# Optimization experiments

Hardware: AMD Instinct MI355X
Metric: run time of the kernel (lower is better)

Reference implementation:

```python
import jax, jax.numpy as jnp
import numpy as np

N1 = 50000
N2 = 50000
E = 800000
D = 128
DOUT = 128
L = 2
NEG_SLOPE = 0.2


def setup_inputs() -> dict:
    key = jax.random.key(0)
    ks = jax.random.split(key, 32)
    s = 0.05
    inp = {
        "x1": jax.random.normal(ks[0], (N1, D), jnp.float32),
        "x2": jax.random.normal(ks[1], (N2, D), jnp.float32),
        "ei11": jax.random.randint(ks[2], (2, E), 0, N1, jnp.int32),
        "ei22": jax.random.randint(ks[3], (2, E), 0, N2, jnp.int32),
        "ei12": jnp.stack([
            jax.random.randint(ks[4], (E,), 0, N1, jnp.int32),
            jax.random.randint(ks[5], (E,), 0, N2, jnp.int32),
        ]),
        # intra protein_1 GATConv params (shared lin for src/dst), stacked over layers
        "W_i1": jax.random.normal(ks[6], (L, D, D), jnp.float32) * s,
        "as_i1": jax.random.normal(ks[7], (L, D), jnp.float32) * s,
        "ad_i1": jax.random.normal(ks[8], (L, D), jnp.float32) * s,
        "b_i1": jnp.zeros((L, D), jnp.float32),
        # intra protein_2
        "W_i2": jax.random.normal(ks[9], (L, D, D), jnp.float32) * s,
        "as_i2": jax.random.normal(ks[10], (L, D), jnp.float32) * s,
        "ad_i2": jax.random.normal(ks[11], (L, D), jnp.float32) * s,
        "b_i2": jnp.zeros((L, D), jnp.float32),
        # inter protein_1 -> protein_2 (bipartite: separate src/dst lin)
        "Ws_x": jax.random.normal(ks[12], (L, D, D), jnp.float32) * s,
        "Wd_x": jax.random.normal(ks[13], (L, D, D), jnp.float32) * s,
        "as_x": jax.random.normal(ks[14], (L, D), jnp.float32) * s,
        "ad_x": jax.random.normal(ks[15], (L, D), jnp.float32) * s,
        "b_x": jnp.zeros((L, D), jnp.float32),
        # final linear
        "W_out": jax.random.normal(ks[16], (D, DOUT), jnp.float32) * s,
        "b_out": jnp.zeros((DOUT,), jnp.float32),
    }
    return inp


def _segment_softmax(logits, seg, num_segments):
    m = jax.ops.segment_max(logits, seg, num_segments=num_segments)
    e = jnp.exp(logits - m[seg])
    z = jax.ops.segment_sum(e, seg, num_segments=num_segments)
    return e / (z[seg] + 1e-16)


def _gat(x_src, x_dst, ei, W_src, W_dst, a_s, a_d, b, num_dst):
    hs = x_src @ W_src                       # [Ns, D]
    hd = x_dst @ W_dst                       # [Nd, D]
    src, dst = ei[0], ei[1]
    logit = jax.nn.leaky_relu((hs @ a_s)[src] + (hd @ a_d)[dst], NEG_SLOPE)  # [E]
    coef = _segment_softmax(logit, dst, num_dst)  # [E]
    out = jax.ops.segment_sum(coef[:, None] * hs[src], dst, num_segments=num_dst)
    return out + b


def reference(x1, x2, ei11, ei22, ei12, W_i1, as_i1, ad_i1, b_i1,
              W_i2, as_i2, ad_i2, b_i2, Ws_x, Wd_x, as_x, ad_x, b_x,
              W_out, b_out):
    h1, h2 = x1, x2
    for l in range(L):
        o1 = _gat(h1, h1, ei11, W_i1[l], W_i1[l], as_i1[l], ad_i1[l], b_i1[l], N1)
        o2 = _gat(h2, h2, ei22, W_i2[l], W_i2[l], as_i2[l], ad_i2[l], b_i2[l], N2)
        o2 = o2 + _gat(h1, h2, ei12, Ws_x[l], Wd_x[l], as_x[l], ad_x[l], b_x[l], N2)
        h1 = jax.nn.relu(o1)
        h2 = jax.nn.relu(o2)
    return (h1 @ W_out + b_out, h2 @ W_out + b_out)
```

## Files before the change

kernel.cpp:

```cpp
#include <hip/hip_runtime.h>
#include <hip/hip_bf16.h>
#include <hip/hip_fp16.h>
#include <cstdint>

#define D 128
#define NEG 0.2f
#define WSH 8
#define WIN 256
#define CAP 5120

typedef _Float16 f16x8 __attribute__((ext_vector_type(8)));
typedef float f32x4 __attribute__((ext_vector_type(4)));

static __device__ __forceinline__ ushort f2h(float x) {
  __half h = __float2half(x);
  return *reinterpret_cast<ushort*>(&h);
}
static __device__ __forceinline__ float h2f(ushort u) {
  __half h = *reinterpret_cast<__half*>(&u);
  return __half2float(h);
}

__global__ __launch_bounds__(256) void bin3_kernel(
    const int* __restrict__ ei0, const int* __restrict__ ei1, const int* __restrict__ ei2,
    int E0, int E1, int E2,
    int* __restrict__ p0, int* __restrict__ p1, int* __restrict__ p2,
    int* __restrict__ bcnt) {
  int sset = blockIdx.y;
  const int* ei = sset == 0 ? ei0 : (sset == 1 ? ei1 : ei2);
  int E = sset == 0 ? E0 : (sset == 1 ? E1 : E2);
  int* pairs = sset == 0 ? p0 : (sset == 1 ? p1 : p2);
  int* bc = bcnt + sset * 256;
  const int* src = ei;
  const int* dst = ei + E;
  __shared__ int lcnt[WIN], lcur[WIN], lbase[WIN];
  int t = threadIdx.x;
  lcnt[t] = 0; lcur[t] = 0;
  __syncthreads();
  int base = blockIdx.x * 2048;
  int s[8], d[8];
  #pragma unroll
  for (int k = 0; k < 8; k++) {
    int e = base + k * 256 + t;
    if (e < E) {
      s[k] = src[e]; d[k] = dst[e];
      atomicAdd(&lcnt[d[k] >> WSH], 1);
    } else d[k] = -1;
  }
  __syncthreads();
  if (lcnt[t] > 0) lbase[t] = atomicAdd(&bc[t], lcnt[t]);
  __syncthreads();
  #pragma unroll
  for (int k = 0; k < 8; k++) {
    if (d[k] >= 0) {
      int b = d[k] >> WSH;
      int r = atomicAdd(&lcur[b], 1);
      int slot = lbase[b] + r;
      if (slot < CAP)
        pairs[(size_t)b * CAP + slot] = (s[k] & 0xFFFF) | ((d[k] & 255) << 16);
    }
  }
}

__global__ __launch_bounds__(256) void count3_kernel(
    const int* __restrict__ p0, const int* __restrict__ p1, const int* __restrict__ p2,
    const int* __restrict__ bcnt,
    int* __restrict__ cnt0, int* __restrict__ cnt1, int* __restrict__ cnt2,
    int* __restrict__ off0, int* __restrict__ off1, int* __restrict__ off2,
    int* __restrict__ wsum, int N0, int N1, int N2) {
  int sset = blockIdx.y;
  const int* pairs = sset == 0 ? p0 : (sset == 1 ? p1 : p2);
  int* cnt = sset == 0 ? cnt0 : (sset == 1 ? cnt1 : cnt2);
  int* offs = sset == 0 ? off0 : (sset == 1 ? off1 : off2);
  int N = sset == 0 ? N0 : (sset == 1 ? N1 : N2);
  const int* bc = bcnt + sset * 256;
  int* ws = wsum + sset * 256;
  __shared__ int h[WIN];
  __shared__ int sc[WIN];
  int b = blockIdx.x, t = threadIdx.x;
  h[t] = 0; __syncthreads();
  int n = bc[b]; if (n > CAP) n = CAP;
  const int* p = pairs + (size_t)b * CAP;
  for (int i = t; i < n; i += 256) atomicAdd(&h[(p[i] >> 16) & 255], 1);
  __syncthreads();
  int v = h[t]; sc[t] = v; __syncthreads();
  for (int o = 1; o < 256; o <<= 1) {
    int x = (t >= o) ? sc[t - o] : 0; __syncthreads();
    sc[t] += x; __syncthreads();
  }
  int node = b * WIN + t;
  if (node < N) { cnt[node] = v; offs[node] = sc[t] - v; }
  if (t == 255) ws[b] = sc[255];
}

__global__ void wscan3_kernel(int* wsum) {
  __shared__ int sc[256];
  int t = threadIdx.x;
  int* w = wsum + blockIdx.x * 256;
  int v = w[t];
  sc[t] = v; __syncthreads();
  for (int o = 1; o < 256; o <<= 1) {
    int x = (t >= o) ? sc[t - o] : 0; __syncthreads();
    sc[t] += x; __syncthreads();
  }
  w[t] = sc[t] - v;
}

__global__ __launch_bounds__(256) void fill23_kernel(
    const int* __restrict__ p0, const int* __restrict__ p1, const int* __restrict__ p2,
    const int* __restrict__ bcnt, const int* __restrict__ wsum,
    int* __restrict__ off0, int* __restrict__ off1, int* __restrict__ off2,
    int* __restrict__ cs0, int* __restrict__ cs1, int* __restrict__ cs2,
    int N0, int N1, int N2) {
  int sset = blockIdx.y;
  const int* pairs = sset == 0 ? p0 : (sset == 1 ? p1 : p2);
  int* offs = sset == 0 ? off0 : (sset == 1 ? off1 : off2);
  int* csrc = sset == 0 ? cs0 : (sset == 1 ? cs1 : cs2);
  int N = sset == 0 ? N0 : (sset == 1 ? N1 : N2);
  const int* bc = bcnt + sset * 256;
  __shared__ int cur[WIN];
  int b = blockIdx.x, t = threadIdx.x;
  int wb = wsum[sset * 256 + b];
  int node = b * WIN + t;
  int start = 0;
  if (node < N) { start = offs[node] + wb; offs[node] = start; }
  cur[t] = start;
  __syncthreads();
  int n = bc[b]; if (n > CAP) n = CAP;
  const int* p = pairs + (size_t)b * CAP;
  for (int i = t; i < n; i += 256) {
    int v = p[i];
    int pp = atomicAdd(&cur[(v >> 16) & 255], 1);
    csrc[pp] = v & 0xFFFF;
  }
}

__global__ __launch_bounds__(256) void wprep6_kernel(
    const float* __restrict__ W_i1, const float* __restrict__ W_i2,
    const float* __restrict__ Ws_x,
    ushort* __restrict__ WtA, ushort* __restrict__ WtB, ushort* __restrict__ WtX) {
  int b = blockIdx.x;
  int which = b >> 1, l = b & 1;
  const float* Wb = (which == 0 ? W_i1 : (which == 1 ? W_i2 : Ws_x)) + l * 16384;
  ushort* Wo = (which == 0 ? WtA : (which == 1 ? WtB : WtX)) + l * 16384;
  __shared__ float s[128 * 129];
  int t = threadIdx.x;
  #pragma unroll
  for (int i = 0; i < 16; i++) {
    int idx = i * 256 + t;
    int k = idx >> 5, n4 = idx & 31;
    float4 v = *(const float4*)&Wb[k * 128 + n4 * 4];
    s[k * 129 + n4 * 4 + 0] = v.x;
    s[k * 129 + n4 * 4 + 1] = v.y;
    s[k * 129 + n4 * 4 + 2] = v.z;
    s[k * 129 + n4 * 4 + 3] = v.w;
  }
  __syncthreads();
  #pragma unroll
  for (int i = 0; i < 8; i++) {
    int idx = i * 256 + t;
    int n = idx >> 4, k8 = (idx & 15) * 8;
    ushort4 h0, h1;
    h0.x = f2h(s[(k8 + 0) * 129 + n]); h0.y = f2h(s[(k8 + 1) * 129 + n]);
    h0.z = f2h(s[(k8 + 2) * 129 + n]); h0.w = f2h(s[(k8 + 3) * 129 + n]);
    h1.x = f2h(s[(k8 + 4) * 129 + n]); h1.y = f2h(s[(k8 + 5) * 129 + n]);
    h1.z = f2h(s[(k8 + 6) * 129 + n]); h1.w = f2h(s[(k8 + 7) * 129 + n]);
    *(ushort4*)&Wo[n * 128 + k8] = h0;
    *(ushort4*)&Wo[n * 128 + k8 + 4] = h1;
  }
}

__global__ __launch_bounds__(256) void wprepout_kernel(
    const float* __restrict__ W, ushort* __restrict__ Wh, ushort* __restrict__ Wl) {
  __shared__ float s[128 * 129];
  int t = threadIdx.x;
  #pragma unroll
  for (int i = 0; i < 16; i++) {
    int idx = i * 256 + t;
    int k = idx >> 5, n4 = idx & 31;
    float4 v = *(const float4*)&W[k * 128 + n4 * 4];
    s[k * 129 + n4 * 4 + 0] = v.x;
    s[k * 129 + n4 * 4 + 1] = v.y;
    s[k * 129 + n4 * 4 + 2] = v.z;
    s[k * 129 + n4 * 4 + 3] = v.w;
  }
  __syncthreads();
  #pragma unroll
  for (int i = 0; i < 8; i++) {
    int idx = i * 256 + t;
    int n = idx >> 4, k8 = (idx & 15) * 8;
    ushort hh[8], ll[8];
    #pragma unroll
    for (int e = 0; e < 8; e++) {
      float w = s[(k8 + e) * 129 + n];
      hh[e] = f2h(w);
      ll[e] = f2h(w - h2f(hh[e]));
    }
    *(ushort4*)&Wh[n * 128 + k8]     = make_ushort4(hh[0], hh[1], hh[2], hh[3]);
    *(ushort4*)&Wh[n * 128 + k8 + 4] = make_ushort4(hh[4], hh[5], hh[6], hh[7]);
    *(ushort4*)&Wl[n * 128 + k8]     = make_ushort4(ll[0], ll[1], ll[2], ll[3]);
    *(ushort4*)&Wl[n * 128 + k8 + 4] = make_ushort4(ll[4], ll[5], ll[6], ll[7]);
  }
}

__global__ void wvec2_kernel(const float* __restrict__ Wd, const float* __restrict__ ad,
                             float* __restrict__ wv) {
  int l = blockIdx.x;
  int r = threadIdx.x;
  const float* Wb = Wd + (size_t)l * 16384;
  const float* ab = ad + l * 128;
  float s = 0.f;
  for (int c = 0; c < D; c++) s += Wb[r * D + c] * ab[c];
  wv[l * 128 + r] = s;
}

#define SWZ(b) ((b) ^ ((((b) >> 8) & 7) << 4))

template <int XF16>
__global__ __launch_bounds__(256) void gemm16_kernel(
    const void* __restrict__ Xv, const ushort* __restrict__ Wt,
    ushort* __restrict__ Yb,
    const float* __restrict__ a_sv, const float* __restrict__ a_dv,
    const float* __restrict__ wvec,
    float* __restrict__ aSo, float* __restrict__ aDo, float* __restrict__ aXo, int M) {
  __shared__ ushort sX[64 * 128];
  __shared__ ushort sW[128 * 128];
  __shared__ float sv[128];
  int t = threadIdx.x;
  int bm = blockIdx.x * 64;
  {
    const uint4* W4 = (const uint4*)Wt;
    #pragma unroll
    for (int i = 0; i < 8; i++) {
      int idx = i * 256 + t;
      int byte = idx * 16;
      *(uint4*)((char*)sW + SWZ(byte)) = W4[idx];
    }
  }
  {
    #pragma unroll
    for (int i = 0; i < 8; i++) {
      int idx = i * 256 + t;
      int row = idx >> 5, c4 = idx & 31;
      ushort4 h = make_ushort4(0, 0, 0, 0);
      if (bm + row < M) {
        if (XF16) {
          h = *(const ushort4*)((const ushort*)Xv + (size_t)(bm + row) * 128 + c4 * 4);
        } else {
          float4 v = ((const float4*)Xv)[(size_t)(bm + row) * 32 + c4];
          h.x = f2h(v.x); h.y = f2h(v.y); h.z = f2h(v.z); h.w = f2h(v.w);
        }
      }
      int byte = idx * 8;
      *(uint2*)((char*)sX + SWZ(byte)) = *(uint2*)&h;
    }
  }
  if (wvec != nullptr && t < 128) sv[t] = wvec[t];
  __syncthreads();

  int w = t >> 6, l = t & 63;
  int lq = l >> 4, lr = l & 15;
  int xrow = w * 16 + lr;
  f32x4 acc[8] = {};
  float ax = 0.f;
  #pragma unroll
  for (int kk = 0; kk < 4; kk++) {
    int xb = xrow * 256 + kk * 64 + lq * 16;
    f16x8 xa = *(const f16x8*)((const char*)sX + SWZ(xb));
    if (wvec != nullptr) {
      float4 w0 = *(const float4*)&sv[kk * 32 + lq * 8];
      float4 w1 = *(const float4*)&sv[kk * 32 + lq * 8 + 4];
      ax += (float)xa[0] * w0.x + (float)xa[1] * w0.y + (float)xa[2] * w0.z + (float)xa[3] * w0.w
          + (float)xa[4] * w1.x + (float)xa[5] * w1.y + (float)xa[6] * w1.z + (float)xa[7] * w1.w;
    }
    #pragma unroll
    for (int ct = 0; ct < 8; ct++) {
      int nb = (ct * 16 + lr) * 256 + kk * 64 + lq * 16;
      f16x8 wa = *(const f16x8*)((const char*)sW + SWZ(nb));
      acc[ct] = __builtin_amdgcn_mfma_f32_16x16x32_f16(wa, xa, acc[ct], 0, 0, 0);
    }
  }
  int row_m = bm + xrow;
  bool valid = row_m < M;
  #pragma unroll
  for (int ct = 0; ct < 8; ct++) {
    ushort4 h;
    h.x = f2h(acc[ct][0]); h.y = f2h(acc[ct][1]);
    h.z = f2h(acc[ct][2]); h.w = f2h(acc[ct][3]);
    if (valid) *(ushort4*)&Yb[(size_t)row_m * 128 + ct * 16 + lq * 4] = h;
  }
  if (a_sv != nullptr) {
    float s = 0.f;
    #pragma unroll
    for (int ct = 0; ct < 8; ct++) {
      float4 a = *(const float4*)&a_sv[ct * 16 + lq * 4];
      s += acc[ct][0] * a.x + acc[ct][1] * a.y + acc[ct][2] * a.z + acc[ct][3] * a.w;
    }
    s += __shfl_xor(s, 16); s += __shfl_xor(s, 32);
    if (valid && lq == 0) aSo[row_m] = s;
  }
  if (a_dv != nullptr) {
    float s = 0.f;
    #pragma unroll
    for (int ct = 0; ct < 8; ct++) {
      float4 a = *(const float4*)&a_dv[ct * 16 + lq * 4];
      s += acc[ct][0] * a.x + acc[ct][1] * a.y + acc[ct][2] * a.z + acc[ct][3] * a.w;
    }
    s += __shfl_xor(s, 16); s += __shfl_xor(s, 32);
    if (valid && lq == 0) aDo[row_m] = s;
  }
  if (wvec != nullptr) {
    ax += __shfl_xor(ax, 16); ax += __shfl_xor(ax, 32);
    if (valid && lq == 0) aXo[row_m] = ax;
  }
}

template <int XF16>
__global__ __launch_bounds__(256) void gemmx2_kernel(
    const void* __restrict__ Xv,
    const ushort* __restrict__ Wt0, const ushort* __restrict__ Wt1,
    ushort* __restrict__ Yb0, ushort* __restrict__ Yb1,
    const float* __restrict__ asv0, const float* __restrict__ asv1,
    const float* __restrict__ adv1,
    float* __restrict__ aSo0, float* __restrict__ aSo1, float* __restrict__ aDo1,
    int M) {
  int y = blockIdx.y;
  const ushort* Wt = y ? Wt1 : Wt0;
  ushort* Yb = y ? Yb1 : Yb0;
  const float* a_sv = y ? asv1 : asv0;
  const float* a_dv = y ? adv1 : nullptr;
  float* aSo = y ? aSo1 : aSo0;
  float* aDo = aDo1;
  __shared__ ushort sX[64 * 128];
  __shared__ ushort sW[128 * 128];
  int t = threadIdx.x;
  int bm = blockIdx.x * 64;
  {
    const uint4* W4 = (const uint4*)Wt;
    #pragma unroll
    for (int i = 0; i < 8; i++) {
      int idx = i * 256 + t;
      int byte = idx * 16;
      *(uint4*)((char*)sW + SWZ(byte)) = W4[idx];
    }
  }
  {
    #pragma unroll
    for (int i = 0; i < 8; i++) {
      int idx = i * 256 + t;
      int row = idx >> 5, c4 = idx & 31;
      ushort4 h = make_ushort4(0, 0, 0, 0);
      if (bm + row < M) {
        if (XF16) {
          h = *(const ushort4*)((const ushort*)Xv + (size_t)(bm + row) * 128 + c4 * 4);
        } else {
          float4 v = ((const float4*)Xv)[(size_t)(bm + row) * 32 + c4];
          h.x = f2h(v.x); h.y = f2h(v.y); h.z = f2h(v.z); h.w = f2h(v.w);
        }
      }
      int byte = idx * 8;
      *(uint2*)((char*)sX + SWZ(byte)) = *(uint2*)&h;
    }
  }
  __syncthreads();
  int w = t >> 6, l = t & 63;
  int lq = l >> 4, lr = l & 15;
  int xrow = w * 16 + lr;
  f32x4 acc[8] = {};
  #pragma unroll
  for (int kk = 0; kk < 4; kk++) {
    int xb = xrow * 256 + kk * 64 + lq * 16;
    f16x8 xa = *(const f16x8*)((const char*)sX + SWZ(xb));
    #pragma unroll
    for (int ct = 0; ct < 8; ct++) {
      int nb = (ct * 16 + lr) * 256 + kk * 64 + lq * 16;
      f16x8 wa = *(const f16x8*)((const char*)sW + SWZ(nb));
      acc[ct] = __builtin_amdgcn_mfma_f32_16x16x32_f16(wa, xa, acc[ct], 0, 0, 0);
    }
  }
  int row_m = bm + xrow;
  bool valid = row_m < M;
  #pragma unroll
  for (int ct = 0; ct < 8; ct++) {
    ushort4 h;
    h.x = f2h(acc[ct][0]); h.y = f2h(acc[ct][1]);
    h.z = f2h(acc[ct][2]); h.w = f2h(acc[ct][3]);
    if (valid) *(ushort4*)&Yb[(size_t)row_m * 128 + ct * 16 + lq * 4] = h;
  }
  {
    float s = 0.f;
    #pragma unroll
    for (int ct = 0; ct < 8; ct++) {
      float4 a = *(const float4*)&a_sv[ct * 16 + lq * 4];
      s += acc[ct][0] * a.x + acc[ct][1] * a.y + acc[ct][2] * a.z + acc[ct][3] * a.w;
    }
    s += __shfl_xor(s, 16); s += __shfl_xor(s, 32);
    if (valid && lq == 0) aSo[row_m] = s;
  }
  if (a_dv != nullptr) {
    float s = 0.f;
    #pragma unroll
    for (int ct = 0; ct < 8; ct++) {
      float4 a = *(const float4*)&a_dv[ct * 16 + lq * 4];
      s += acc[ct][0] * a.x + acc[ct][1] * a.y + acc[ct][2] * a.z + acc[ct][3] * a.w;
    }
    s += __shfl_xor(s, 16); s += __shfl_xor(s, 32);
    if (valid && lq == 0) aDo[row_m] = s;
  }
}

__global__ __launch_bounds__(512) void gemmfin_kernel(
    const float* __restrict__ XA, const float* __restrict__ XB,
    const ushort* __restrict__ Wh, const ushort* __restrict__ Wl,
    const float* __restrict__ bias,
    float* __restrict__ YA, float* __restrict__ YB, int MA, int MB, int mgA) {
  int bid = blockIdx.x;
  const float* X; float* Y; int M, bm;
  if (bid < mgA) { X = XA; Y = YA; M = MA; bm = bid * 128; }
  else           { X = XB; Y = YB; M = MB; bm = (bid - mgA) * 128; }
  __shared__ ushort sWh[128 * 128];
  __shared__ ushort sWl[128 * 128];
  __shared__ ushort sH[128 * 128];
  __shared__ ushort sL[128 * 128];
  int t = threadIdx.x;
  {
    const uint4* Wh4 = (const uint4*)Wh;
    const uint4* Wl4 = (const uint4*)Wl;
    #pragma unroll
    for (int i = 0; i < 4; i++) {
      int idx = i * 512 + t;
      int byte = idx * 16;
      *(uint4*)((char*)sWh + SWZ(byte)) = Wh4[idx];
      *(uint4*)((char*)sWl + SWZ(byte)) = Wl4[idx];
    }
  }
  {
    const float4* X4 = (const float4*)X;
    #pragma unroll
    for (int i = 0; i < 8; i++) {
      int idx = i * 512 + t;
      int row = idx >> 5, c4 = idx & 31;
      float4 v = make_float4(0.f, 0.f, 0.f, 0.f);
      if (bm + row < M) v = X4[(size_t)(bm + row) * 32 + c4];
      ushort4 h, lo;
      h.x = f2h(v.x); lo.x = f2h(v.x - h2f(h.x));
      h.y = f2h(v.y); lo.y = f2h(v.y - h2f(h.y));
      h.z = f2h(v.z); lo.z = f2h(v.z - h2f(h.z));
      h.w = f2h(v.w); lo.w = f2h(v.w - h2f(h.w));
      int byte = idx * 8;
      *(uint2*)((char*)sH + SWZ(byte)) = *(uint2*)&h;
      *(uint2*)((char*)sL + SWZ(byte)) = *(uint2*)&lo;
    }
  }
  __syncthreads();
  int w = t >> 6, l = t & 63;
  int lq = l >> 4, lr = l & 15;
  int xrow = w * 16 + lr;
  f32x4 acc[8] = {};
  #pragma unroll
  for (int kk = 0; kk < 4; kk++) {
    int xb = xrow * 256 + kk * 64 + lq * 16;
    f16x8 xh = *(const f16x8*)((const char*)sH + SWZ(xb));
    f16x8 xl = *(const f16x8*)((const char*)sL + SWZ(xb));
    #pragma unroll
    for (int ct = 0; ct < 8; ct++) {
      int nb = (ct * 16 + lr) * 256 + kk * 64 + lq * 16;
      f16x8 wh = *(const f16x8*)((const char*)sWh + SWZ(nb));
      f16x8 wl = *(const f16x8*)((const char*)sWl + SWZ(nb));
      acc[ct] = __builtin_amdgcn_mfma_f32_16x16x32_f16(wh, xh, acc[ct], 0, 0, 0);
      acc[ct] = __builtin_amdgcn_mfma_f32_16x16x32_f16(wl, xh, acc[ct], 0, 0, 0);
      acc[ct] = __builtin_amdgcn_mfma_f32_16x16x32_f16(wh, xl, acc[ct], 0, 0, 0);
    }
  }
  int row_m = bm + xrow;
  if (row_m < M) {
    #pragma unroll
    for (int ct = 0; ct < 8; ct++) {
      float4 b = *(const float4*)&bias[ct * 16 + lq * 4];
      float4 o = make_float4(acc[ct][0] + b.x, acc[ct][1] + b.y,
                             acc[ct][2] + b.z, acc[ct][3] + b.w);
      *(float4*)&Y[(size_t)row_m * 128 + ct * 16 + lq * 4] = o;
    }
  }
}

template <int F16O>
__global__ __launch_bounds__(256) void agg_kernel(
    const ushort* __restrict__ hs, const float* __restrict__ aS, const float* __restrict__ aD,
    const int* __restrict__ offs, const int* __restrict__ cnt, const int* __restrict__ csrc,
    const void* __restrict__ prevv, const float* __restrict__ bias1,
    const float* __restrict__ bias2, void* __restrict__ outv, int N, int dorelu) {
  int wid = threadIdx.x >> 6, lane = threadIdx.x & 63;
  int d = blockIdx.x * 4 + wid;
  if (d >= N) return;
  int st = offs[d], deg = cnt[d];
  float adv = aD[d];
  int quarter = lane >> 4;
  int q = lane & 15;
  float acc[8] = {};
  float z = 0.f;
  for (int base = 0; base < deg; base += 64) {
    int m = deg - base; if (m > 64) m = 64;
    int sidx = 0; float el = 0.f;
    if (lane < m) {
      sidx = csrc[st + base + lane];
      float l = aS[sidx] + adv;
      l = (l > 0.f) ? l : NEG * l;
      el = __expf(l);
    }
    float zs = el;
    for (int o = 32; o > 0; o >>= 1) zs += __shfl_xor(zs, o);
    z += zs;
    #pragma unroll 4
    for (int j = 0; j < m; j += 4) {
      int jj = j + quarter;
      int sj = __shfl(sidx, jj);
      float ej = __shfl(el, jj);
      uint4 hv = *(const uint4*)(hs + (size_t)sj * D + q * 8);
      float2 f0 = __half22float2(*reinterpret_cast<__half2*>(&hv.x));
      float2 f1 = __half22float2(*reinterpret_cast<__half2*>(&hv.y));
      float2 f2 = __half22float2(*reinterpret_cast<__half2*>(&hv.z));
      float2 f3 = __half22float2(*reinterpret_cast<__half2*>(&hv.w));
      acc[0] += ej * f0.x; acc[1] += ej * f0.y;
      acc[2] += ej * f1.x; acc[3] += ej * f1.y;
      acc[4] += ej * f2.x; acc[5] += ej * f2.y;
      acc[6] += ej * f3.x; acc[7] += ej * f3.y;
    }
  }
  #pragma unroll
  for (int k = 0; k < 8; k++) {
    acc[k] += __shfl_xor(acc[k], 16);
    acc[k] += __shfl_xor(acc[k], 32);
  }
  if (quarter == 0) {
    float inv = 1.f / (z + 1e-16f);
    float o[8];
    #pragma unroll
    for (int k = 0; k < 8; k++) o[k] = acc[k] * inv;
    size_t rb = (size_t)d * D + q * 8;
    if (prevv) {
      if (F16O) {
        uint4 pv = *(const uint4*)((const ushort*)prevv + rb);
        float2 p0 = __half22float2(*reinterpret_cast<__half2*>(&pv.x));
        float2 p1 = __half22float2(*reinterpret_cast<__half2*>(&pv.y));
        float2 p2 = __half22float2(*reinterpret_cast<__half2*>(&pv.z));
        float2 p3 = __half22float2(*reinterpret_cast<__half2*>(&pv.w));
        o[0]+=p0.x; o[1]+=p0.y; o[2]+=p1.x; o[3]+=p1.y;
        o[4]+=p2.x; o[5]+=p2.y; o[6]+=p3.x; o[7]+=p3.y;
      } else {
        const float* prev = (const float*)prevv;
        float4 p0 = *(const float4*)(prev + rb);
        float4 p1 = *(const float4*)(prev + rb + 4);
        o[0]+=p0.x; o[1]+=p0.y; o[2]+=p0.z; o[3]+=p0.w;
        o[4]+=p1.x; o[5]+=p1.y; o[6]+=p1.z; o[7]+=p1.w;
      }
    }
    if (bias1) {
      float4 b0 = *(const float4*)(bias1 + q * 8);
      float4 b1 = *(const float4*)(bias1 + q * 8 + 4);
      o[0]+=b0.x; o[1]+=b0.y; o[2]+=b0.z; o[3]+=b0.w;
      o[4]+=b1.x; o[5]+=b1.y; o[6]+=b1.z; o[7]+=b1.w;
    }
    if (bias2) {
      float4 b0 = *(const float4*)(bias2 + q * 8);
      float4 b1 = *(const float4*)(bias2 + q * 8 + 4);
      o[0]+=b0.x; o[1]+=b0.y; o[2]+=b0.z; o[3]+=b0.w;
      o[4]+=b1.x; o[5]+=b1.y; o[6]+=b1.z; o[7]+=b1.w;
    }
    if (dorelu) {
      #pragma unroll
      for (int k = 0; k < 8; k++) o[k] = o[k] > 0.f ? o[k] : 0.f;
    }
    if (F16O) {
      ushort4 u0 = make_ushort4(f2h(o[0]), f2h(o[1]), f2h(o[2]), f2h(o[3]));
      ushort4 u1 = make_ushort4(f2h(o[4]), f2h(o[5]), f2h(o[6]), f2h(o[7]));
      *(ushort4*)((ushort*)outv + rb)     = u0;
      *(ushort4*)((ushort*)outv + rb + 4) = u1;
    } else {
      float* out = (float*)outv;
      *(float4*)(out + rb)     = make_float4(o[0], o[1], o[2], o[3]);
      *(float4*)(out + rb + 4) = make_float4(o[4], o[5], o[6], o[7]);
    }
  }
}

extern "C" void kernel_launch(void* const* d_in, const int* in_sizes, int n_in,
                              void* d_out, int out_size, void* d_ws, size_t ws_size,
                              hipStream_t stream) {
  const float* x1   = (const float*)d_in[0];
  const float* x2   = (const float*)d_in[1];
  const int*   ei11 = (const int*)d_in[2];
  const int*   ei22 = (const int*)d_in[3];
  const int*   ei12 = (const int*)d_in[4];
  const float* W_i1 = (const float*)d_in[5];
  const float* as_i1= (const float*)d_in[6];
  const float* ad_i1= (const float*)d_in[7];
  const float* b_i1 = (const float*)d_in[8];
  const float* W_i2 = (const float*)d_in[9];
  const float* as_i2= (const float*)d_in[10];
  const float* ad_i2= (const float*)d_in[11];
  const float* b_i2 = (const float*)d_in[12];
  const float* Ws_x = (const float*)d_in[13];
  const float* Wd_x = (const float*)d_in[14];
  const float* as_x = (const float*)d_in[15];
  const float* ad_x = (const float*)d_in[16];
  const float* b_x  = (const float*)d_in[17];
  const float* W_out= (const float*)d_in[18];
  const float* b_out= (const float*)d_in[19];

  int N1 = in_sizes[0] / D, N2 = in_sizes[1] / D;
  int E11 = in_sizes[2] / 2, E22 = in_sizes[3] / 2, E12 = in_sizes[4] / 2;
  int Nmax = (N1 > N2) ? N1 : N2;
  int Emax = E11 > E22 ? (E11 > E12 ? E11 : E12) : (E22 > E12 ? E22 : E12);
  int NB1 = (N1 + WIN - 1) / WIN, NB2 = (N2 + WIN - 1) / WIN;
  int NBmax = (NB1 > NB2) ? NB1 : NB2;

  float* outA = (float*)d_out;
  float* outB = outA + (size_t)N1 * D;

  char* w = (char*)d_ws;
  auto alloc = [&](size_t b) { char* p = w; w += (b + 255) & ~(size_t)255; return p; };
  size_t pair_bytes = (size_t)NBmax * CAP * 4;
  size_t hsmax = (size_t)Nmax * D * 2;
  ushort* BB  = (ushort*)alloc(hsmax > pair_bytes ? hsmax : pair_bytes);
  ushort* BX  = (ushort*)alloc(hsmax > pair_bytes ? hsmax : pair_bytes);
  ushort* h1  = (ushort*)alloc(((size_t)N1 * D * 2) > pair_bytes ? ((size_t)N1 * D * 2) : pair_bytes);
  ushort* h2  = (ushort*)alloc((size_t)N2 * D * 2);
  int* pairs0 = (int*)BB;
  int* pairs1 = (int*)BX;
  int* pairs2 = (int*)h1;
  float* aS   = (float*)alloc((size_t)Nmax * 4);
  float* aD   = (float*)alloc((size_t)Nmax * 4);
  float* aDx  = (float*)alloc((size_t)Nmax * 4);
  float* aS2  = (float*)alloc((size_t)Nmax * 4);
  float* wvecB= (float*)alloc(256 * 4);
  ushort* WtA = (ushort*)alloc(2 * 16384 * 2);
  ushort* WtB = (ushort*)alloc(2 * 16384 * 2);
  ushort* WtX = (ushort*)alloc(2 * 16384 * 2);
  ushort* Wfh = (ushort*)alloc(16384 * 2);
  ushort* Wfl = (ushort*)alloc(16384 * 2);
  int* bcnt  = (int*)alloc(3 * 256 * 4);
  int* wsum  = (int*)alloc(3 * 256 * 4);
  int* cnt11 = (int*)alloc((size_t)N1 * 4);
  int* off11 = (int*)alloc((size_t)N1 * 4);
  int* csA   = (int*)alloc((size_t)E11 * 4);
  int* cnt22 = (int*)alloc((size_t)N2 * 4);
  int* off22 = (int*)alloc((size_t)N2 * 4);
  int* csB   = (int*)alloc((size_t)E22 * 4);
  int* cnt12 = (int*)alloc((size_t)N2 * 4);
  int* off12 = (int*)alloc((size_t)N2 * 4);
  int* csC   = (int*)alloc((size_t)E12 * 4);

  hipMemsetAsync(bcnt, 0, 3 * 256 * 4, stream);
  bin3_kernel<<<dim3((Emax + 2047) / 2048, 3), 256, 0, stream>>>(
      ei11, ei22, ei12, E11, E22, E12, pairs0, pairs1, pairs2, bcnt);
  count3_kernel<<<dim3(NBmax, 3), 256, 0, stream>>>(
      pairs0, pairs1, pairs2, bcnt, cnt11, cnt22, cnt12,
      off11, off22, off12, wsum, N1, N2, N2);
  wscan3_kernel<<<3, 256, 0, stream>>>(wsum);
  fill23_kernel<<<dim3(NBmax, 3), 256, 0, stream>>>(
      pairs0, pairs1, pairs2, bcnt, wsum, off11, off22, off12,
      csA, csB, csC, N1, N2, N2);

  wprep6_kernel<<<6, 256, 0, stream>>>(W_i1, W_i2, Ws_x, WtA, WtB, WtX);
  wprepout_kernel<<<1, 256, 0, stream>>>(W_out, Wfh, Wfl);
  wvec2_kernel<<<2, 128, 0, stream>>>(Wd_x, ad_x, wvecB);

  int mg1 = (N1 + 63) / 64, mg2 = (N2 + 63) / 64;
  int fg1 = (N1 + 127) / 128, fg2 = (N2 + 127) / 128;
  int gg1 = (N1 + 3) / 4, gg2 = (N2 + 3) / 4;
  ushort* hsB = BB;
  ushort* hsX = BX;
  ushort* hsA = BB;

  gemm16_kernel<0><<<mg2, 256, 0, stream>>>(x2, WtB, hsB,
      as_i2, ad_i2, wvecB, aS, aD, aDx, N2);
  agg_kernel<1><<<gg2, 256, 0, stream>>>(hsB, aS, aD, off22, cnt22, csB,
      nullptr, b_i2, b_x, h2, N2, 0);
  gemmx2_kernel<0><<<dim3(mg1, 2), 256, 0, stream>>>(x1, WtX, WtA, hsX, hsA,
      as_x, as_i1, ad_i1, aS2, aS, aD, N1);
  agg_kernel<1><<<gg2, 256, 0, stream>>>(hsX, aS2, aDx, off12, cnt12, csC,
      h2, nullptr, nullptr, h2, N2, 1);
  agg_kernel<1><<<gg1, 256, 0, stream>>>(hsA, aS, aD, off11, cnt11, csA,
      nullptr, b_i1, nullptr, h1, N1, 1);

  gemm16_kernel<1><<<mg2, 256, 0, stream>>>(h2, WtB + 16384, hsB,
      as_i2 + 128, ad_i2 + 128, wvecB + 128, aS, aD, aDx, N2);
  agg_kernel<0><<<gg2, 256, 0, stream>>>(hsB, aS, aD, off22, cnt22, csB,
      nullptr, b_i2 + 128, b_x + 128, outB, N2, 0);
  gemmx2_kernel<1><<<dim3(mg1, 2), 256, 0, stream>>>(h1, WtX + 16384, WtA + 16384,
      hsX, hsA, as_x + 128, as_i1 + 128, ad_i1 + 128, aS2, aS, aD, N1);
  agg_kernel<0><<<gg2, 256, 0, stream>>>(hsX, aS2, aDx, off12, cnt12, csC,
      outB, nullptr, nullptr, outB, N2, 1);
  agg_kernel<0><<<gg1, 256, 0, stream>>>(hsA, aS, aD, off11, cnt11, csA,
      nullptr, b_i1 + 128, nullptr, outA, N1, 1);

  gemmfin_kernel<<<fg1 + fg2, 512, 0, stream>>>(outA, outB, Wfh, Wfl, b_out,
                                                outA, outB, N1, N2, fg1);
}
```

Measured before the change: 420.4 us.

## Fuse intra and inter aggregations, compact CSR indices to 16-bit, fp16 final GEMM input

Merges the protein_2 intra and cross-graph aggregations into one kernel that gathers both edge sets per destination and writes the summed, biased, ReLU'd fp16 result directly. This removes an extra read-modify-write pass over h2 and one launch per layer. CSR source indices are stored as ushort instead of int, halving index traffic. Layer-2 outputs are kept in fp16, so the final GEMM reads half-width input and drops the low-part split MFMA, trading some precision for less traffic and compute. Kernel order is reshuffled so the protein_1 aggregation follows its GEMM, reusing buffers.

```diff
diff --git a/kernel.cpp b/kernel.cpp
--- a/kernel.cpp
+++ b/kernel.cpp
@@ -110,12 +110,12 @@
     const int* __restrict__ p0, const int* __restrict__ p1, const int* __restrict__ p2,
     const int* __restrict__ bcnt, const int* __restrict__ wsum,
     int* __restrict__ off0, int* __restrict__ off1, int* __restrict__ off2,
-    int* __restrict__ cs0, int* __restrict__ cs1, int* __restrict__ cs2,
+    ushort* __restrict__ cs0, ushort* __restrict__ cs1, ushort* __restrict__ cs2,
     int N0, int N1, int N2) {
   int sset = blockIdx.y;
   const int* pairs = sset == 0 ? p0 : (sset == 1 ? p1 : p2);
   int* offs = sset == 0 ? off0 : (sset == 1 ? off1 : off2);
-  int* csrc = sset == 0 ? cs0 : (sset == 1 ? cs1 : cs2);
+  ushort* csrc = sset == 0 ? cs0 : (sset == 1 ? cs1 : cs2);
   int N = sset == 0 ? N0 : (sset == 1 ? N1 : N2);
   const int* bc = bcnt + sset * 256;
   __shared__ int cur[WIN];
@@ -131,7 +131,7 @@
   for (int i = t; i < n; i += 256) {
     int v = p[i];
     int pp = atomicAdd(&cur[(v >> 16) & 255], 1);
-    csrc[pp] = v & 0xFFFF;
+    csrc[pp] = (ushort)(v & 0xFFFF);
   }
 }
 
@@ -410,18 +410,17 @@
 }
 
 __global__ __launch_bounds__(512) void gemmfin_kernel(
-    const float* __restrict__ XA, const float* __restrict__ XB,
+    const ushort* __restrict__ XA, const ushort* __restrict__ XB,
     const ushort* __restrict__ Wh, const ushort* __restrict__ Wl,
     const float* __restrict__ bias,
     float* __restrict__ YA, float* __restrict__ YB, int MA, int MB, int mgA) {
   int bid = blockIdx.x;
-  const float* X; float* Y; int M, bm;
+  const ushort* X; float* Y; int M, bm;
   if (bid < mgA) { X = XA; Y = YA; M = MA; bm = bid * 128; }
   else           { X = XB; Y = YB; M = MB; bm = (bid - mgA) * 128; }
   __shared__ ushort sWh[128 * 128];
   __shared__ ushort sWl[128 * 128];
   __shared__ ushort sH[128 * 128];
-  __shared__ ushort sL[128 * 128];
   int t = threadIdx.x;
   {
     const uint4* Wh4 = (const uint4*)Wh;
@@ -435,21 +434,14 @@
     }
   }
   {
-    const float4* X4 = (const float4*)X;
-    #pragma unroll
-    for (int i = 0; i < 8; i++) {
+    const uint4* X4 = (const uint4*)X;
+    #pragma unroll
+    for (int i = 0; i < 4; i++) {
       int idx = i * 512 + t;
-      int row = idx >> 5, c4 = idx & 31;
-      float4 v = make_float4(0.f, 0.f, 0.f, 0.f);
-      if (bm + row < M) v = X4[(size_t)(bm + row) * 32 + c4];
-      ushort4 h, lo;
-      h.x = f2h(v.x); lo.x = f2h(v.x - h2f(h.x));
-      h.y = f2h(v.y); lo.y = f2h(v.y - h2f(h.y));
-      h.z = f2h(v.z); lo.z = f2h(v.z - h2f(h.z));
-      h.w = f2h(v.w); lo.w = f2h(v.w - h2f(h.w));
-      int byte = idx * 8;
-      *(uint2*)((char*)sH + SWZ(byte)) = *(uint2*)&h;
-      *(uint2*)((char*)sL + SWZ(byte)) = *(uint2*)&lo;
+      int row = idx >> 4, c8 = idx & 15;
+      uint4 v = make_uint4(0, 0, 0, 0);
+      if (bm + row < M) v = X4[(size_t)(bm + row) * 16 + c8];
+      *(uint4*)((char*)sH + SWZ(idx * 16)) = v;
     }
   }
   __syncthreads();
@@ -461,7 +453,6 @@
   for (int kk = 0; kk < 4; kk++) {
     int xb = xrow * 256 + kk * 64 + lq * 16;
     f16x8 xh = *(const f16x8*)((const char*)sH + SWZ(xb));
-    f16x8 xl = *(const f16x8*)((const char*)sL + SWZ(xb));
     #pragma unroll
     for (int ct = 0; ct < 8; ct++) {
       int nb = (ct * 16 + lr) * 256 + kk * 64 + lq * 16;
@@ -469,7 +460,6 @@
       f16x8 wl = *(const f16x8*)((const char*)sWl + SWZ(nb));
       acc[ct] = __builtin_amdgcn_mfma_f32_16x16x32_f16(wh, xh, acc[ct], 0, 0, 0);
       acc[ct] = __builtin_amdgcn_mfma_f32_16x16x32_f16(wl, xh, acc[ct], 0, 0, 0);
-      acc[ct] = __builtin_amdgcn_mfma_f32_16x16x32_f16(wh, xl, acc[ct], 0, 0, 0);
     }
   }
   int row_m = bm + xrow;
@@ -484,27 +474,16 @@
   }
 }
 
-template <int F16O>
-__global__ __launch_bounds__(256) void agg_kernel(
-    const ushort* __restrict__ hs, const float* __restrict__ aS, const float* __restrict__ aD,
-    const int* __restrict__ offs, const int* __restrict__ cnt, const int* __restrict__ csrc,
-    const void* __restrict__ prevv, const float* __restrict__ bias1,
-    const float* __restrict__ bias2, void* __restrict__ outv, int N, int dorelu) {
-  int wid = threadIdx.x >> 6, lane = threadIdx.x & 63;
-  int d = blockIdx.x * 4 + wid;
-  if (d >= N) return;
-  int st = offs[d], deg = cnt[d];
-  float adv = aD[d];
-  int quarter = lane >> 4;
-  int q = lane & 15;
-  float acc[8] = {};
-  float z = 0.f;
+static __device__ __forceinline__ void gather_rows(
+    const ushort* __restrict__ hs, const float* __restrict__ aSv, float adv,
+    int st, int deg, const ushort* __restrict__ cs,
+    int lane, int quarter, int q, float acc[8], float& z) {
   for (int base = 0; base < deg; base += 64) {
     int m = deg - base; if (m > 64) m = 64;
     int sidx = 0; float el = 0.f;
     if (lane < m) {
-      sidx = csrc[st + base + lane];
-      float l = aS[sidx] + adv;
+      sidx = cs[st + base + lane];
+      float l = aSv[sidx] + adv;
       l = (l > 0.f) ? l : NEG * l;
       el = __expf(l);
     }
@@ -527,60 +506,77 @@
       acc[6] += ej * f3.x; acc[7] += ej * f3.y;
     }
   }
+}
+
+__global__ __launch_bounds__(256) void agg1_kernel(
+    const ushort* __restrict__ hs, const float* __restrict__ aS, const float* __restrict__ aD,
+    const int* __restrict__ offs, const int* __restrict__ cnt, const ushort* __restrict__ csrc,
+    const float* __restrict__ bias1, ushort* __restrict__ out, int N) {
+  int wid = threadIdx.x >> 6, lane = threadIdx.x & 63;
+  int d = blockIdx.x * 4 + wid;
+  if (d >= N) return;
+  int quarter = lane >> 4, q = lane & 15;
+  float acc[8] = {}; float z = 0.f;
+  gather_rows(hs, aS, aD[d], offs[d], cnt[d], csrc, lane, quarter, q, acc, z);
+  float inv = 1.f / (z + 1e-16f);
+  float res[8];
+  #pragma unroll
+  for (int k = 0; k < 8; k++) res[k] = acc[k] * inv;
   #pragma unroll
   for (int k = 0; k < 8; k++) {
-    acc[k] += __shfl_xor(acc[k], 16);
-    acc[k] += __shfl_xor(acc[k], 32);
+    res[k] += __shfl_xor(res[k], 16);
+    res[k] += __shfl_xor(res[k], 32);
   }
   if (quarter == 0) {
-    float inv = 1.f / (z + 1e-16f);
-    float o[8];
-    #pragma unroll
-    for (int k = 0; k < 8; k++) o[k] = acc[k] * inv;
+    float4 b0 = *(const float4*)(bias1 + q * 8);
+    float4 b1 = *(const float4*)(bias1 + q * 8 + 4);
+    res[0]+=b0.x; res[1]+=b0.y; res[2]+=b0.z; res[3]+=b0.w;
+    res[4]+=b1.x; res[5]+=b1.y; res[6]+=b1.z; res[7]+=b1.w;
+    #pragma unroll
+    for (int k = 0; k < 8; k++) res[k] = res[k] > 0.f ? res[k] : 0.f;
     size_t rb = (size_t)d * D + q * 8;
-    if (prevv) {
-      if (F16O) {
-        uint4 pv = *(const uint4*)((const ushort*)prevv + rb);
-        float2 p0 = __half22float2(*reinterpret_cast<__half2*>(&pv.x));
-        float2 p1 = __half22float2(*reinterpret_cast<__half2*>(&pv.y));
-        float2 p2 = __half22float2(*reinterpret_cast<__half2*>(&pv.z));
-        float2 p3 = __half22float2(*reinterpret_cast<__half2*>(&pv.w));
-        o[0]+=p0.x; o[1]+=p0.y; o[2]+=p1.x; o[3]+=p1.y;
-        o[4]+=p2.x; o[5]+=p2.y; o[6]+=p3.x; o[7]+=p3.y;
-      } else {
-        const float* prev = (const float*)prevv;
-        float4 p0 = *(const float4*)(prev + rb);
-        float4 p1 = *(const float4*)(prev + rb + 4);
-        o[0]+=p0.x; o[1]+=p0.y; o[2]+=p0.z; o[3]+=p0.w;
-        o[4]+=p1.x; o[5]+=p1.y; o[6]+=p1.z; o[7]+=p1.w;
-      }
-    }
-    if (bias1) {
-      float4 b0 = *(const float4*)(bias1 + q * 8);
-      float4 b1 = *(const float4*)(bias1 + q * 8 + 4);
-      o[0]+=b0.x; o[1]+=b0.y; o[2]+=b0.z; o[3]+=b0.w;
-      o[4]+=b1.x; o[5]+=b1.y; o[6]+=b1.z; o[7]+=b1.w;
-    }
-    if (bias2) {
-      float4 b0 = *(const float4*)(bias2 + q * 8);
-      float4 b1 = *(const float4*)(bias2 + q * 8 + 4);
-      o[0]+=b0.x; o[1]+=b0.y; o[2]+=b0.z; o[3]+=b0.w;
-      o[4]+=b1.x; o[5]+=b1.y; o[6]+=b1.z; o[7]+=b1.w;
-    }
-    if (dorelu) {
-      #pragma unroll
-      for (int k = 0; k < 8; k++) o[k] = o[k] > 0.f ? o[k] : 0.f;
-    }
-    if (F16O) {
-      ushort4 u0 = make_ushort4(f2h(o[0]), f2h(o[1]), f2h(o[2]), f2h(o[3]));
-      ushort4 u1 = make_ushort4(f2h(o[4]), f2h(o[5]), f2h(o[6]), f2h(o[7]));
-      *(ushort4*)((ushort*)outv + rb)     = u0;
-      *(ushort4*)((ushort*)outv + rb + 4) = u1;
-    } else {
-      float* out = (float*)outv;
-      *(float4*)(out + rb)     = make_float4(o[0], o[1], o[2], o[3]);
-      *(float4*)(out + rb + 4) = make_float4(o[4], o[5], o[6], o[7]);
-    }
+    *(ushort4*)(out + rb)     = make_ushort4(f2h(res[0]), f2h(res[1]), f2h(res[2]), f2h(res[3]));
+    *(ushort4*)(out + rb + 4) = make_ushort4(f2h(res[4]), f2h(res[5]), f2h(res[6]), f2h(res[7]));
+  }
+}
+
+__global__ __launch_bounds__(256) void agg2_kernel(
+    const ushort* __restrict__ hs1, const float* __restrict__ aS1, const float* __restrict__ aD1,
+    const int* __restrict__ off1, const int* __restrict__ cnt1, const ushort* __restrict__ cs1,
+    const ushort* __restrict__ hs2, const float* __restrict__ aS2v, const float* __restrict__ aD2v,
+    const int* __restrict__ off2, const int* __restrict__ cnt2, const ushort* __restrict__ cs2,
+    const float* __restrict__ bias1, const float* __restrict__ bias2,
+    ushort* __restrict__ out, int N) {
+  int wid = threadIdx.x >> 6, lane = threadIdx.x & 63;
+  int d = blockIdx.x * 4 + wid;
+  if (d >= N) return;
+  int quarter = lane >> 4, q = lane & 15;
+  float acc1[8] = {}; float z1 = 0.f;
+  gather_rows(hs1, aS1, aD1[d], off1[d], cnt1[d], cs1, lane, quarter, q, acc1, z1);
+  float acc2[8] = {}; float z2 = 0.f;
+  gather_rows(hs2, aS2v, aD2v[d], off2[d], cnt2[d], cs2, lane, quarter, q, acc2, z2);
+  float inv1 = 1.f / (z1 + 1e-16f);
+  float inv2 = 1.f / (z2 + 1e-16f);
+  float res[8];
+  #pragma unroll
+  for (int k = 0; k < 8; k++) res[k] = acc1[k] * inv1 + acc2[k] * inv2;
+  #pragma unroll
+  for (int k = 0; k < 8; k++) {
+    res[k] += __shfl_xor(res[k], 16);
+    res[k] += __shfl_xor(res[k], 32);
+  }
+  if (quarter == 0) {
+    float4 b0 = *(const float4*)(bias1 + q * 8);
+    float4 b1 = *(const float4*)(bias1 + q * 8 + 4);
+    float4 c0 = *(const float4*)(bias2 + q * 8);
+    float4 c1 = *(const float4*)(bias2 + q * 8 + 4);
+    res[0]+=b0.x+c0.x; res[1]+=b0.y+c0.y; res[2]+=b0.z+c0.z; res[3]+=b0.w+c0.w;
+    res[4]+=b1.x+c1.x; res[5]+=b1.y+c1.y; res[6]+=b1.z+c1.z; res[7]+=b1.w+c1.w;
+    #pragma unroll
+    for (int k = 0; k < 8; k++) res[k] = res[k] > 0.f ? res[k] : 0.f;
+    size_t rb = (size_t)d * D + q * 8;
+    *(ushort4*)(out + rb)     = make_ushort4(f2h(res[0]), f2h(res[1]), f2h(res[2]), f2h(res[3]));
+    *(ushort4*)(out + rb + 4) = make_ushort4(f2h(res[4]), f2h(res[5]), f2h(res[6]), f2h(res[7]));
   }
 }
 
@@ -643,13 +639,13 @@
   int* wsum  = (int*)alloc(3 * 256 * 4);
   int* cnt11 = (int*)alloc((size_t)N1 * 4);
   int* off11 = (int*)alloc((size_t)N1 * 4);
-  int* csA   = (int*)alloc((size_t)E11 * 4);
+  ushort* csA = (ushort*)alloc((size_t)E11 * 2);
   int* cnt22 = (int*)alloc((size_t)N2 * 4);
   int* off22 = (int*)alloc((size_t)N2 * 4);
-  int* csB   = (int*)alloc((size_t)E22 * 4);
+  ushort* csB = (ushort*)alloc((size_t)E22 * 2);
   int* cnt12 = (int*)alloc((size_t)N2 * 4);
   int* off12 = (int*)alloc((size_t)N2 * 4);
-  int* csC   = (int*)alloc((size_t)E12 * 4);
+  ushort* csC = (ushort*)alloc((size_t)E12 * 2);
 
   hipMemsetAsync(bcnt, 0, 3 * 256 * 4, stream);
   bin3_kernel<<<dim3((Emax + 2047) / 2048, 3), 256, 0, stream>>>(
@@ -669,32 +665,27 @@
   int mg1 = (N1 + 63) / 64, mg2 = (N2 + 63) / 64;
   int fg1 = (N1 + 127) / 128, fg2 = (N2 + 127) / 128;
   int gg1 = (N1 + 3) / 4, gg2 = (N2 + 3) / 4;
+  ushort* hsA = BB;
   ushort* hsB = BB;
   ushort* hsX = BX;
-  ushort* hsA = BB;
-
+
+  gemmx2_kernel<0><<<dim3(mg1, 2), 256, 0, stream>>>(x1, WtX, WtA, hsX, hsA,
+      as_x, as_i1, ad_i1, aS2, aS, aD, N1);
+  agg1_kernel<<<gg1, 256, 0, stream>>>(hsA, aS, aD, off11, cnt11, csA, b_i1, h1, N1);
   gemm16_kernel<0><<<mg2, 256, 0, stream>>>(x2, WtB, hsB,
       as_i2, ad_i2, wvecB, aS, aD, aDx, N2);
-  agg_kernel<1><<<gg2, 256, 0, stream>>>(hsB, aS, aD, off22, cnt22, csB,
-      nullptr, b_i2, b_x, h2, N2, 0);
-  gemmx2_kernel<0><<<dim3(mg1, 2), 256, 0, stream>>>(x1, WtX, WtA, hsX, hsA,
-      as_x, as_i1, ad_i1, aS2, aS, aD, N1);
-  agg_kernel<1><<<gg2, 256, 0, stream>>>(hsX, aS2, aDx, off12, cnt12, csC,
-      h2, nullptr, nullptr, h2, N2, 1);
-  agg_kernel<1><<<gg1, 256, 0, stream>>>(hsA, aS, aD, off11, cnt11, csA,
-      nullptr, b_i1, nullptr, h1, N1, 1);
-
+  agg2_kernel<<<gg2, 256, 0, stream>>>(hsB, aS, aD, off22, cnt22, csB,
+      hsX, aS2, aDx, off12, cnt12, csC, b_i2, b_x, h2, N2);
+
+  gemmx2_kernel<1><<<dim3(mg1, 2), 256, 0, stream>>>(h1, WtX + 16384, WtA + 16384,
+      hsX, hsA, as_x + 128, as_i1 + 128, ad_i1 + 128, aS2, aS, aD, N1);
+  agg1_kernel<<<gg1, 256, 0, stream>>>(hsA, aS, aD, off11, cnt11, csA,
+      b_i1 + 128, h1, N1);
   gemm16_kernel<1><<<mg2, 256, 0, stream>>>(h2, WtB + 16384, hsB,
       as_i2 + 128, ad_i2 + 128, wvecB + 128, aS, aD, aDx, N2);
-  agg_kernel<0><<<gg2, 256, 0, stream>>>(hsB, aS, aD, off22, cnt22, csB,
-      nullptr, b_i2 + 128, b_x + 128, outB, N2, 0);
-  gemmx2_kernel<1><<<dim3(mg1, 2), 256, 0, stream>>>(h1, WtX + 16384, WtA + 16384,
-      hsX, hsA, as_x + 128, as_i1 + 128, ad_i1 + 128, aS2, aS, aD, N1);
-  agg_kernel<0><<<gg2, 256, 0, stream>>>(hsX, aS2, aDx, off12, cnt12, csC,
-      outB, nullptr, nullptr, outB, N2, 1);
-  agg_kernel<0><<<gg1, 256, 0, stream>>>(hsA, aS, aD, off11, cnt11, csA,
-      nullptr, b_i1 + 128, nullptr, outA, N1, 1);
-
-  gemmfin_kernel<<<fg1 + fg2, 512, 0, stream>>>(outA, outB, Wfh, Wfl, b_out,
+  agg2_kernel<<<gg2, 256, 0, stream>>>(hsB, aS, aD, off22, cnt22, csB,
+      hsX, aS2, aDx, off12, cnt12, csC, b_i2 + 128, b_x + 128, h2, N2);
+
+  gemmfin_kernel<<<fg1 + fg2, 512, 0, stream>>>(h1, h2, Wfh, Wfl, b_out,
                                                 outA, outB, N1, N2, fg1);
 }
```

Result: faster. 384.0 us (-8.7%).
